# Performance work log

Measured on AMD Instinct MI355X. Metric: run time of the kernel, lower is better.

Reference implementation:

```python
import jax, jax.numpy as jnp
import numpy as np

B, C, H, W = 16, 256, 96, 96


def setup_inputs() -> dict:
    key = jax.random.key(0)
    ks = jax.random.split(key, 10)
    s = 1.0 / np.sqrt(C)
    return {
        "x": jax.random.normal(ks[0], (B, C, H, W), dtype=jnp.float32) * 0.1,
        "w_theta": jax.random.normal(ks[1], (C, C), dtype=jnp.float32) * s,
        "b_theta": jax.random.normal(ks[2], (C,), dtype=jnp.float32) * 0.01,
        "w_phi": jax.random.normal(ks[3], (C, C), dtype=jnp.float32) * s,
        "b_phi": jax.random.normal(ks[4], (C,), dtype=jnp.float32) * 0.01,
        "w_g": jax.random.normal(ks[5], (C, C), dtype=jnp.float32) * s,
        "b_g": jax.random.normal(ks[6], (C,), dtype=jnp.float32) * 0.01,
        "beta_w": jax.random.normal(ks[7], (), dtype=jnp.float32) * 0.1,
        "beta_h": jax.random.normal(ks[8], (), dtype=jnp.float32) * 0.1,
        "beta_c": jax.random.normal(ks[9], (), dtype=jnp.float32) * 0.1,
    }


def _conv1x1(x, w, b):
    # 1x1 conv == channel mixing: [B,C,H,W] x [O,C] -> [B,O,H,W]
    return jnp.einsum('bchw,oc->bohw', x, w) + b[None, :, None, None]


def _axis_att(q, k, v, perm):
    # perm maps [B,C,H,W] -> [B, axis, rest...]; attention over `axis`
    qp = jnp.transpose(q, perm)
    kp = jnp.transpose(k, perm)
    vp = jnp.transpose(v, perm)
    shp = vp.shape
    n = shp[1]
    qf = qp.reshape(shp[0], n, -1)
    kf = kp.reshape(shp[0], n, -1)
    vf = vp.reshape(shp[0], n, -1)
    att = jax.nn.softmax(jnp.einsum('bik,bjk->bij', qf, kf), axis=-1)  # [B,n,n]
    out = jnp.einsum('bij,bjk->bik', att, vf).reshape(shp)
    inv = np.argsort(perm)
    return jnp.transpose(out, inv)


def reference(x, w_theta, b_theta, w_phi, b_phi, w_g, b_g, beta_w, beta_h, beta_c):
    # width: perm (0,3,2,1); height: (0,2,1,3); channel: (0,1,2,3)
    perms = [(0, 3, 2, 1), (0, 2, 1, 3), (0, 1, 2, 3)]
    betas = [beta_w, beta_h, beta_c]
    for perm, beta in zip(perms, betas):
        theta_x = _conv1x1(x, w_theta, b_theta)
        phi_x = _conv1x1(x, w_phi, b_phi)
        g_x = _conv1x1(x, w_g, b_g)
        x_t = _axis_att(theta_x, phi_x, g_x, perm)
        x = x + x_t * beta
    return x
```

## Files before the change

### kernel.cpp

```cpp
#include <hip/hip_runtime.h>
#include <hip/hip_bf16.h>

using bf16 = __hip_bfloat16;
using short8 = __attribute__((ext_vector_type(8))) short;
using float4v = __attribute__((ext_vector_type(4))) float;

#define BM 64
#define BN 64
#define BK 32
#define LDSP 40

__device__ inline short f2b(float x) {
  bf16 h = __float2bfloat16(x);
  return __builtin_bit_cast(short, h);
}

__device__ inline int swz(int row, int g) { return (g ^ ((row >> 3) & 3)) * 8; }

template<int F32>
__device__ inline short8 ld8e(const void* base, long eoff) {
  short8 r;
  if constexpr (F32) {
    const float* f = (const float*)base + eoff;
    #pragma unroll
    for (int i = 0; i < 8; ++i) r[i] = f2b(f[i]);
  } else {
    r = *(const short8*)((const short*)base + eoff);
  }
  return r;
}

template<int AF, int BF, int EPI, int AF32, int BF32>
__global__ __launch_bounds__(256) void gemm_k(
    const void* __restrict__ Ag, const void* __restrict__ Bg,
    void* __restrict__ Cv, void* __restrict__ Cv2, const float* __restrict__ bias,
    const float* __restrict__ betaP, const float* __restrict__ resid,
    short* __restrict__ xbout,
    int M, int N, int K, int lda, int ldb, int ldc,
    long sA, long sB, long sC, int ksplit, int abdiv, int msplit, int swapxy)
{
  constexpr int SMEM_SHORTS = (EPI >= 4) ? (64 * 68 * 2) : ((BM + BN) * LDSP);
  __shared__ __align__(16) short smem[SMEM_SHORTS];
  short (*As)[LDSP] = (short (*)[LDSP])smem;
  short (*Bs)[LDSP] = (short (*)[LDSP])(smem + BM * LDSP);
  const int t = threadIdx.x;
  const int lane = t & 63;
  const int wave = t >> 6;
  const int wm = (wave >> 1) * 32;
  const int wn = (wave & 1) * 32;
  const int fr = lane & 15;
  const int fq = lane >> 4;
  const int bz = blockIdx.z;
  const int batch = bz / ksplit;
  const int kc = bz - batch * ksplit;
  const int Kc = K / ksplit;
  const int k0 = kc * Kc;
  int bxi = blockIdx.x, byi = blockIdx.y;
  if (swapxy) { int tmp = bxi; bxi = byi; byi = tmp; }
  const int tm0 = byi * BM;
  const int tn0 = bxi * BN;
  const long abase = (long)(batch / abdiv) * sA;
  const long bbase = (long)batch * sB;

  float4v acc[2][2] = {};

  for (int kk = 0; kk < Kc; kk += BK) {
    const int kbase = k0 + kk;
    if constexpr (AF == 0 || AF == 2) {
      int m = t >> 2;
      int kloc = (t & 3) * 8;
      int gk = kbase + kloc;
      short8 v = {};
      if (tm0 + m < M) {
        long off;
        if constexpr (AF == 0) off = abase + (long)(tm0 + m) * lda + gk;
        else                   off = abase + (long)(gk / 96) * 9216 + (long)(tm0 + m) * 96 + (gk % 96);
        v = ld8e<AF32>(Ag, off);
      }
      *(short8*)&As[m][swz(m, t & 3)] = v;
    } else {
      int m = t & 63;
      int kg = t >> 6;
      short8 v = {};
      if (tm0 + m < M) {
        #pragma unroll
        for (int j = 0; j < 8; ++j) {
          long off = abase + (long)(kbase + kg * 8 + j) * lda + tm0 + m;
          v[j] = AF32 ? f2b(((const float*)Ag)[off]) : ((const short*)Ag)[off];
        }
      }
      *(short8*)&As[m][swz(m, kg)] = v;
    }
    if constexpr (BF == 0 || BF == 2) {
      int n = t >> 2;
      int kloc = (t & 3) * 8;
      int gk = kbase + kloc;
      short8 v = {};
      if (tn0 + n < N) {
        long off;
        if constexpr (BF == 0) off = bbase + (long)(tn0 + n) * ldb + gk;
        else                   off = bbase + (long)(gk / 96) * 9216 + (long)(tn0 + n) * 96 + (gk % 96);
        v = ld8e<BF32>(Bg, off);
      }
      *(short8*)&Bs[n][swz(n, t & 3)] = v;
    } else {
      int n = t & 63;
      int kg = t >> 6;
      short8 v = {};
      if (tn0 + n < N) {
        #pragma unroll
        for (int j = 0; j < 8; ++j) {
          long off = bbase + (long)(kbase + kg * 8 + j) * ldb + tn0 + n;
          v[j] = BF32 ? f2b(((const float*)Bg)[off]) : ((const short*)Bg)[off];
        }
      }
      *(short8*)&Bs[n][swz(n, kg)] = v;
    }
    __syncthreads();
    short8 af[2], bfv[2];
    #pragma unroll
    for (int i = 0; i < 2; ++i) { int r = wm + i * 16 + fr; af[i] = *(const short8*)&As[r][swz(r, fq)]; }
    #pragma unroll
    for (int j = 0; j < 2; ++j) { int r = wn + j * 16 + fr; bfv[j] = *(const short8*)&Bs[r][swz(r, fq)]; }
    #pragma unroll
    for (int i = 0; i < 2; ++i)
      #pragma unroll
      for (int j = 0; j < 2; ++j)
        acc[i][j] = __builtin_amdgcn_mfma_f32_16x16x32_bf16(af[i], bfv[j], acc[i][j], 0, 0, 0);
    __syncthreads();
  }

  float beta = 0.0f;
  if constexpr (EPI >= 2) beta = *betaP;
  const long cb = (long)batch * sC;

  if constexpr (EPI == 1) {
    short* Cb = (short*)Cv;
    int rbase = tm0;
    if (Cv2 != nullptr && tm0 >= msplit) { Cb = (short*)Cv2; rbase = tm0 - msplit; }
    short (*Ct)[72] = (short (*)[72])smem;
    #pragma unroll
    for (int i = 0; i < 2; ++i)
      #pragma unroll
      for (int j = 0; j < 2; ++j)
        #pragma unroll
        for (int r = 0; r < 4; ++r) {
          int row = wm + i * 16 + fq * 4 + r;
          int col = wn + j * 16 + fr;
          float v = acc[i][j][r];
          if (bias) v += bias[tm0 + row];
          Ct[row][col] = f2b(v);
        }
    __syncthreads();
    const bool full = (tm0 + BM <= M) && (tn0 + BN <= N);
    #pragma unroll
    for (int rr = 0; rr < 2; ++rr) {
      int row = rr * 32 + (t >> 3);
      int c8 = (t & 7) * 8;
      if (full) {
        *(short8*)(Cb + cb + (long)(rbase + row) * ldc + tn0 + c8) = *(const short8*)&Ct[row][c8];
      } else if (tm0 + row < M) {
        #pragma unroll
        for (int e = 0; e < 8; ++e)
          if (tn0 + c8 + e < N)
            Cb[cb + (long)(rbase + row) * ldc + tn0 + c8 + e] = Ct[row][c8 + e];
      }
    }
  } else if constexpr (EPI >= 4) {
    float (*Cf)[68] = (float (*)[68])smem;
    #pragma unroll
    for (int i = 0; i < 2; ++i)
      #pragma unroll
      for (int j = 0; j < 2; ++j)
        #pragma unroll
        for (int r = 0; r < 4; ++r)
          Cf[wm + i * 16 + fq * 4 + r][wn + j * 16 + fr] = acc[i][j][r];
    __syncthreads();
    int row = t >> 2;
    int seg = (t & 3) * 16;
    int grow = tm0 + row;
    if (grow < M && seg < N - tn0) {
      float* xp = (float*)Cv;
      long base = cb + (long)grow * ldc + tn0 + seg;
      float4v nv[4];
      #pragma unroll
      for (int q = 0; q < 4; ++q) {
        float4v xv;
        if constexpr (EPI == 4) xv = *(const float4v*)(xp + base + q * 4);
        else                    xv = *(const float4v*)(resid + base + q * 4);
        #pragma unroll
        for (int e = 0; e < 4; ++e) nv[q][e] = xv[e] + beta * Cf[row][seg + q * 4 + e];
        *(float4v*)(xp + base + q * 4) = nv[q];
      }
      if (xbout) {
        short8 s0, s1;
        #pragma unroll
        for (int e = 0; e < 4; ++e) { s0[e] = f2b(nv[0][e]); s0[e + 4] = f2b(nv[1][e]); }
        #pragma unroll
        for (int e = 0; e < 4; ++e) { s1[e] = f2b(nv[2][e]); s1[e + 4] = f2b(nv[3][e]); }
        *(short8*)(xbout + base) = s0;
        *(short8*)(xbout + base + 8) = s1;
      }
    }
  } else {
    #pragma unroll
    for (int i = 0; i < 2; ++i) {
      #pragma unroll
      for (int j = 0; j < 2; ++j) {
        #pragma unroll
        for (int r = 0; r < 4; ++r) {
          int row = tm0 + wm + i * 16 + fq * 4 + r;
          int col = tn0 + wn + j * 16 + fr;
          if (row < M && col < N)
            atomicAdd((float*)Cv + cb + (long)row * ldc + col, acc[i][j][r]);
        }
      }
    }
  }
}

__global__ __launch_bounds__(256) void cvt_k(
    const float* __restrict__ in, short* __restrict__ out, long n)
{
  long i = ((long)blockIdx.x * 256 + threadIdx.x) * 8;
  if (i >= n) return;
  const float4v* p = (const float4v*)(in + i);
  float4v a = p[0], b = p[1];
  short8 v;
  v[0] = f2b(a[0]); v[1] = f2b(a[1]); v[2] = f2b(a[2]); v[3] = f2b(a[3]);
  v[4] = f2b(b[0]); v[5] = f2b(b[1]); v[6] = f2b(b[2]); v[7] = f2b(b[3]);
  *(short8*)(out + i) = v;
}

__global__ __launch_bounds__(256) void softmax_k(
    const float* __restrict__ in, short* __restrict__ out, int n, int rows,
    const float* __restrict__ addj, const float* __restrict__ rowv,
    const float* __restrict__ colv)
{
  int wave = threadIdx.x >> 6;
  int lane = threadIdx.x & 63;
  int row = blockIdx.x * 4 + wave;
  if (row >= rows) return;
  int b = row / n;
  const float* r = in + (long)row * n;
  float rv = rowv ? rowv[row] : 0.0f;
  float vals[4];
  float m = -1e30f;
  #pragma unroll
  for (int i = 0; i < 4; ++i) {
    int c = lane + i * 64;
    float v = -1e30f;
    if (c < n) {
      v = r[c];
      if (addj) v += addj[(long)b * n + c];
      if (colv) v += rv * colv[c];
    }
    vals[i] = v;
    m = fmaxf(m, v);
  }
  #pragma unroll
  for (int off = 32; off > 0; off >>= 1) m = fmaxf(m, __shfl_xor(m, off));
  float s = 0.0f;
  #pragma unroll
  for (int i = 0; i < 4; ++i) {
    int c = lane + i * 64;
    float e = (c < n) ? __expf(vals[i] - m) : 0.0f;
    vals[i] = e;
    s += e;
  }
  #pragma unroll
  for (int off = 32; off > 0; off >>= 1) s += __shfl_xor(s, off);
  float inv = 1.0f / s;
  #pragma unroll
  for (int i = 0; i < 4; ++i) {
    int c = lane + i * 64;
    if (c < n) out[(long)row * n + c] = f2b(vals[i] * inv);
  }
}

__global__ __launch_bounds__(256) void sum_rows_k(
    const short* __restrict__ src, float* __restrict__ dst, int rowlen, int nrows)
{
  int wave = threadIdx.x >> 6;
  int lane = threadIdx.x & 63;
  int row = blockIdx.x * 4 + wave;
  if (row >= nrows) return;
  const short* p = src + (long)row * rowlen;
  float s = 0.0f;
  for (int k = lane; k < rowlen; k += 64)
    s += __bfloat162float(__builtin_bit_cast(bf16, p[k]));
  #pragma unroll
  for (int off = 32; off > 0; off >>= 1) s += __shfl_xor(s, off);
  if (lane == 0) dst[row] = s;
}

__global__ __launch_bounds__(256) void wv_k(
    const float* __restrict__ wphi, const float* __restrict__ btheta, float* __restrict__ wv)
{
  int c = threadIdx.x;
  float s = 0.0f;
  for (int o = 0; o < 256; ++o) s += btheta[o] * wphi[o * 256 + c];
  wv[c] = s;
}

__global__ __launch_bounds__(256) void vfull_k(
    const float* __restrict__ x, const float* __restrict__ wv, float* __restrict__ vf)
{
  long idx = (long)blockIdx.x * 256 + threadIdx.x;
  int b = (int)(idx / 9216);
  int hw = (int)(idx % 9216);
  const float* p = x + (long)b * 2359296 + hw;
  float s = 0.0f;
  for (int c = 0; c < 256; ++c) s += wv[c] * p[(long)c * 9216];
  vf[idx] = s;
}

__global__ __launch_bounds__(256) void rsum_k(
    const float* __restrict__ vf, float* __restrict__ r, int axis)
{
  int idx = blockIdx.x * 256 + threadIdx.x;
  int b = idx / 96;
  int j = idx % 96;
  const float* p = vf + (long)b * 9216;
  float s = 0.0f;
  if (axis == 0) { for (int h = 0; h < 96; ++h) s += p[h * 96 + j]; }
  else           { for (int w = 0; w < 96; ++w) s += p[j * 96 + w]; }
  r[idx] = s;
}

__global__ __launch_bounds__(256) void fill_k(
    const float* __restrict__ wth, const float* __restrict__ wg,
    const float* __restrict__ bth, const float* __restrict__ bg,
    short* __restrict__ st1, short* __restrict__ st2,
    float* __restrict__ b1, float* __restrict__ b2)
{
  int r = blockIdx.x, c = threadIdx.x;
  if (r < 256) {
    st2[r * 256 + c] = f2b(wth[r * 256 + c]);
  } else {
    short v = f2b(wg[(r - 256) * 256 + c]);
    st1[r * 256 + c] = v;
    st2[r * 256 + c] = v;
  }
  if (r == 0) { b1[c] = 0.0f; b2[c] = bth[c]; }
  if (r == 1) { b1[256 + c] = bg[c]; b2[256 + c] = bg[c]; }
}

extern "C" void kernel_launch(void* const* d_in, const int* in_sizes, int n_in,
                              void* d_out, int out_size, void* d_ws, size_t ws_size,
                              hipStream_t stream)
{
  const long TS = 37748736L;
  const long BS = 2359296L;
  const size_t POOL = 12u * 1024 * 1024;

  float* x = (float*)d_out;
  const float* xin = (const float*)d_in[0];
  const float* wth = (const float*)d_in[1];
  const float* bth = (const float*)d_in[2];
  const float* wph = (const float*)d_in[3];
  const float* bph = (const float*)d_in[4];
  const float* wg  = (const float*)d_in[5];
  const float* bg  = (const float*)d_in[6];
  const float* beta_w = (const float*)d_in[7];
  const float* beta_h = (const float*)d_in[8];
  const float* beta_c = (const float*)d_in[9];

  const size_t need_full = (size_t)6 * TS + POOL;
  const bool full = ws_size >= need_full;

  short* xb   = (short*)d_ws;
  short* bigY = xb + TS;
  char*  pool = (char*)(bigY + TS);
  short* bigG = full ? (short*)(pool + POOL) : bigY;
  float* attf  = (float*)pool;
  short* attb  = (short*)(attf + 1048576);
  float* Zf    = (float*)(attb + 1048576);
  short* st1   = (short*)(Zf + 1048576);
  short* st2   = st1 + 131072;
  float* bias1 = (float*)(st2 + 131072);
  float* bias2 = bias1 + 512;
  float* vfull = bias2 + 512;
  float* rbuf  = vfull + 147456;
  float* wv    = rbuf + 1536;
  float* tbar  = wv + 256;

  dim3 blk(256);

  gemm_k<1,1,1,1,1><<<dim3(4,4,1), blk, 0, stream>>>(wth, wph, st1, nullptr, nullptr, nullptr, nullptr,
      nullptr, 256, 256, 256, 256, 256, 256, 0, 0, 0, 1, 1, 0, 0);
  fill_k<<<512, blk, 0, stream>>>(wth, wg, bth, bg, st1, st2, bias1, bias2);
  wv_k<<<1, blk, 0, stream>>>(wph, bth, wv);
  cvt_k<<<18432, blk, 0, stream>>>(xin, xb, TS);

  for (int pass = 0; pass < 2; ++pass) {
    const float* xs = (pass == 0) ? xin : (const float*)x;
    if (full) {
      gemm_k<0,1,1,0,0><<<dim3(144,8,16), blk, 0, stream>>>(st1, xb, bigY, bigG, bias1, nullptr, nullptr,
          nullptr, 512, 9216, 256, 256, 9216, 9216, 0, BS, BS, 1, 1, 256, 0);
    } else {
      gemm_k<0,1,1,0,0><<<dim3(144,4,16), blk, 0, stream>>>(st1, xb, bigY, nullptr, nullptr, nullptr, nullptr,
          nullptr, 256, 9216, 256, 256, 9216, 9216, 0, BS, BS, 1, 1, 0, 0);
    }
    vfull_k<<<576, blk, 0, stream>>>(xs, wv, vfull);
    rsum_k<<<6, blk, 0, stream>>>(vfull, rbuf, pass);
    hipMemsetAsync(attf, 0, (size_t)16 * 9216 * sizeof(float), stream);
    if (pass == 0)
      gemm_k<1,1,0,0,0><<<dim3(2,2,256), blk, 0, stream>>>(xb, bigY, attf, nullptr, nullptr, nullptr, nullptr,
          nullptr, 96, 96, 24576, 96, 96, 96, BS, BS, 9216, 16, 1, 0, 0);
    else
      gemm_k<2,2,0,0,0><<<dim3(2,2,256), blk, 0, stream>>>(xb, bigY, attf, nullptr, nullptr, nullptr, nullptr,
          nullptr, 96, 96, 24576, 0, 0, 96, BS, BS, 9216, 16, 1, 0, 0);
    softmax_k<<<384, blk, 0, stream>>>(attf, attb, 96, 1536, rbuf, nullptr, nullptr);
    if (!full) {
      gemm_k<0,1,1,0,0><<<dim3(144,4,16), blk, 0, stream>>>(st1 + 65536, xb, bigG, nullptr, bias1 + 256,
          nullptr, nullptr, nullptr, 256, 9216, 256, 256, 9216, 9216, 0, BS, BS, 1, 1, 0, 0);
    }
    if (pass == 0)
      gemm_k<0,0,5,0,0><<<dim3(2,384,16), blk, 0, stream>>>(bigG, attb, x, nullptr, nullptr, beta_w, xin,
          xb, 24576, 96, 96, 96, 96, 96, BS, 9216, BS, 1, 1, 0, 0);
    else
      gemm_k<0,1,4,0,0><<<dim3(2,2,4096), blk, 0, stream>>>(attb, bigG, x, nullptr, nullptr, beta_h, nullptr,
          xb, 96, 96, 96, 96, 96, 96, 9216, 9216, 9216, 1, 256, 0, 0);
  }

  if (full) {
    gemm_k<0,1,1,0,0><<<dim3(144,8,16), blk, 0, stream>>>(st2, xb, bigY, bigG, bias2, nullptr, nullptr,
        nullptr, 512, 9216, 256, 256, 9216, 9216, 0, BS, BS, 1, 1, 256, 0);
  } else {
    gemm_k<0,1,1,0,0><<<dim3(144,4,16), blk, 0, stream>>>(st2, xb, bigY, nullptr, bias2, nullptr, nullptr,
        nullptr, 256, 9216, 256, 256, 9216, 9216, 0, BS, BS, 1, 1, 0, 0);
  }
  hipMemsetAsync(Zf, 0, (size_t)16 * 256 * 256 * sizeof(float), stream);
  gemm_k<0,0,0,0,0><<<dim3(4,4,64), blk, 0, stream>>>(bigY, xb, Zf, nullptr, nullptr, nullptr, nullptr,
      nullptr, 256, 256, 9216, 9216, 9216, 256, BS, BS, 65536, 4, 1, 0, 0);
  sum_rows_k<<<1024, blk, 0, stream>>>(bigY, tbar, 9216, 4096);
  hipMemsetAsync(attf, 0, (size_t)16 * 256 * 256 * sizeof(float), stream);
  gemm_k<0,0,0,1,1><<<dim3(4,4,16), blk, 0, stream>>>(Zf, wph, attf, nullptr, nullptr, nullptr, nullptr,
      nullptr, 256, 256, 256, 256, 256, 256, 65536, 0, 65536, 1, 1, 0, 0);
  softmax_k<<<1024, blk, 0, stream>>>(attf, attb, 256, 4096, nullptr, tbar, bph);
  if (!full) {
    gemm_k<0,1,1,0,0><<<dim3(144,4,16), blk, 0, stream>>>(st1 + 65536, xb, bigG, nullptr, bias1 + 256,
        nullptr, nullptr, nullptr, 256, 9216, 256, 256, 9216, 9216, 0, BS, BS, 1, 1, 0, 0);
  }
  gemm_k<0,1,4,0,0><<<dim3(144,4,16), blk, 0, stream>>>(attb, bigG, x, nullptr, nullptr, beta_c, nullptr,
      nullptr, 256, 9216, 256, 256, 9216, 9216, 65536, BS, BS, 1, 1, 0, 0);
}
```

Before: 1.445 ms.

## Compute channel attention via Gram matrix of x instead of theta projection

The channel-attention logits theta·phiᵀ are re-associated as Wθ·(X Xᵀ)·Wφᵀ plus bias terms built from per-channel sums of x. The large theta projection GEMM over all pixels is replaced by a 256x256 Gram GEMM per batch followed by small weight GEMMs. The per-channel sums are accumulated with atomics inside the preceding height-pass epilogue, and rank-one bias corrections are folded into the initial logits. This drops the K=9216 projection and the row-sum kernel, at the cost of extra small kernels and a different rounding path through bf16 Gram storage.

Result: no change. 1.441 ms (-0.3%).

```diff
diff --git a/kernel.cpp b/kernel.cpp
--- a/kernel.cpp
+++ b/kernel.cpp
@@ -35,7 +35,7 @@
     const void* __restrict__ Ag, const void* __restrict__ Bg,
     void* __restrict__ Cv, void* __restrict__ Cv2, const float* __restrict__ bias,
     const float* __restrict__ betaP, const float* __restrict__ resid,
-    short* __restrict__ xbout,
+    short* __restrict__ xbout, float* __restrict__ xbarP,
     int M, int N, int K, int lda, int ldb, int ldc,
     long sA, long sB, long sC, int ksplit, int abdiv, int msplit, int swapxy)
 {
@@ -179,6 +179,7 @@
     int row = t >> 2;
     int seg = (t & 3) * 16;
     int grow = tm0 + row;
+    float part = 0.0f;
     if (grow < M && seg < N - tn0) {
       float* xp = (float*)Cv;
       long base = cb + (long)grow * ldc + tn0 + seg;
@@ -189,7 +190,7 @@
         if constexpr (EPI == 4) xv = *(const float4v*)(xp + base + q * 4);
         else                    xv = *(const float4v*)(resid + base + q * 4);
         #pragma unroll
-        for (int e = 0; e < 4; ++e) nv[q][e] = xv[e] + beta * Cf[row][seg + q * 4 + e];
+        for (int e = 0; e < 4; ++e) { nv[q][e] = xv[e] + beta * Cf[row][seg + q * 4 + e]; part += nv[q][e]; }
         *(float4v*)(xp + base + q * 4) = nv[q];
       }
       if (xbout) {
@@ -201,6 +202,11 @@
         *(short8*)(xbout + base) = s0;
         *(short8*)(xbout + base + 8) = s1;
       }
+    }
+    if (xbarP) {
+      #pragma unroll
+      for (int off = 32; off > 0; off >>= 1) part += __shfl_xor(part, off);
+      if (lane == 0) atomicAdd(&xbarP[batch], part);
     }
   } else {
     #pragma unroll
@@ -278,22 +284,6 @@
   }
 }
 
-__global__ __launch_bounds__(256) void sum_rows_k(
-    const short* __restrict__ src, float* __restrict__ dst, int rowlen, int nrows)
-{
-  int wave = threadIdx.x >> 6;
-  int lane = threadIdx.x & 63;
-  int row = blockIdx.x * 4 + wave;
-  if (row >= nrows) return;
-  const short* p = src + (long)row * rowlen;
-  float s = 0.0f;
-  for (int k = lane; k < rowlen; k += 64)
-    s += __bfloat162float(__builtin_bit_cast(bf16, p[k]));
-  #pragma unroll
-  for (int off = 32; off > 0; off >>= 1) s += __shfl_xor(s, off);
-  if (lane == 0) dst[row] = s;
-}
-
 __global__ __launch_bounds__(256) void wv_k(
     const float* __restrict__ wphi, const float* __restrict__ btheta, float* __restrict__ wv)
 {
@@ -326,6 +316,32 @@
   if (axis == 0) { for (int h = 0; h < 96; ++h) s += p[h * 96 + j]; }
   else           { for (int w = 0; w < 96; ++w) s += p[j * 96 + w]; }
   r[idx] = s;
+}
+
+__global__ __launch_bounds__(256) void tq_k(
+    const float* __restrict__ wth, const float* __restrict__ bth,
+    const float* __restrict__ wph, const float* __restrict__ xbar,
+    float* __restrict__ tbar, float* __restrict__ q)
+{
+  int b = blockIdx.x, i = threadIdx.x;
+  const float* xb_ = xbar + b * 256;
+  float s1 = 0.0f, s2 = 0.0f;
+  for (int k = 0; k < 256; ++k) {
+    s1 += wth[i * 256 + k] * xb_[k];
+    s2 += wph[i * 256 + k] * xb_[k];
+  }
+  tbar[b * 256 + i] = s1 + 9216.0f * bth[i];
+  q[b * 256 + i] = s2;
+}
+
+__global__ __launch_bounds__(256) void initL_k(
+    const float* __restrict__ tbar, const float* __restrict__ q,
+    const float* __restrict__ bth, const float* __restrict__ bph,
+    float* __restrict__ attf)
+{
+  int bi = blockIdx.x;
+  int b = bi >> 8, i = bi & 255, j = threadIdx.x;
+  attf[(long)bi * 256 + j] = tbar[bi] * bph[j] + bth[i] * q[b * 256 + j];
 }
 
 __global__ __launch_bounds__(256) void fill_k(
@@ -384,65 +400,62 @@
   float* rbuf  = vfull + 147456;
   float* wv    = rbuf + 1536;
   float* tbar  = wv + 256;
+  float* xbar  = tbar + 4096;
+  float* qv    = xbar + 4096;
+  short* Sb    = attb;
+  short* Ztb   = (short*)Zf;
 
   dim3 blk(256);
 
   gemm_k<1,1,1,1,1><<<dim3(4,4,1), blk, 0, stream>>>(wth, wph, st1, nullptr, nullptr, nullptr, nullptr,
-      nullptr, 256, 256, 256, 256, 256, 256, 0, 0, 0, 1, 1, 0, 0);
+      nullptr, nullptr, 256, 256, 256, 256, 256, 256, 0, 0, 0, 1, 1, 0, 0);
   fill_k<<<512, blk, 0, stream>>>(wth, wg, bth, bg, st1, st2, bias1, bias2);
   wv_k<<<1, blk, 0, stream>>>(wph, bth, wv);
   cvt_k<<<18432, blk, 0, stream>>>(xin, xb, TS);
+  hipMemsetAsync(xbar, 0, 4096 * sizeof(float), stream);
 
   for (int pass = 0; pass < 2; ++pass) {
     const float* xs = (pass == 0) ? xin : (const float*)x;
     if (full) {
       gemm_k<0,1,1,0,0><<<dim3(144,8,16), blk, 0, stream>>>(st1, xb, bigY, bigG, bias1, nullptr, nullptr,
-          nullptr, 512, 9216, 256, 256, 9216, 9216, 0, BS, BS, 1, 1, 256, 0);
+          nullptr, nullptr, 512, 9216, 256, 256, 9216, 9216, 0, BS, BS, 1, 1, 256, 0);
     } else {
       gemm_k<0,1,1,0,0><<<dim3(144,4,16), blk, 0, stream>>>(st1, xb, bigY, nullptr, nullptr, nullptr, nullptr,
-          nullptr, 256, 9216, 256, 256, 9216, 9216, 0, BS, BS, 1, 1, 0, 0);
+          nullptr, nullptr, 256, 9216, 256, 256, 9216, 9216, 0, BS, BS, 1, 1, 0, 0);
     }
     vfull_k<<<576, blk, 0, stream>>>(xs, wv, vfull);
     rsum_k<<<6, blk, 0, stream>>>(vfull, rbuf, pass);
     hipMemsetAsync(attf, 0, (size_t)16 * 9216 * sizeof(float), stream);
     if (pass == 0)
       gemm_k<1,1,0,0,0><<<dim3(2,2,256), blk, 0, stream>>>(xb, bigY, attf, nullptr, nullptr, nullptr, nullptr,
-          nullptr, 96, 96, 24576, 96, 96, 96, BS, BS, 9216, 16, 1, 0, 0);
+          nullptr, nullptr, 96, 96, 24576, 96, 96, 96, BS, BS, 9216, 16, 1, 0, 0);
     else
       gemm_k<2,2,0,0,0><<<dim3(2,2,256), blk, 0, stream>>>(xb, bigY, attf, nullptr, nullptr, nullptr, nullptr,
-          nullptr, 96, 96, 24576, 0, 0, 96, BS, BS, 9216, 16, 1, 0, 0);
+          nullptr, nullptr, 96, 96, 24576, 0, 0, 96, BS, BS, 9216, 16, 1, 0, 0);
     softmax_k<<<384, blk, 0, stream>>>(attf, attb, 96, 1536, rbuf, nullptr, nullptr);
     if (!full) {
       gemm_k<0,1,1,0,0><<<dim3(144,4,16), blk, 0, stream>>>(st1 + 65536, xb, bigG, nullptr, bias1 + 256,
-          nullptr, nullptr, nullptr, 256, 9216, 256, 256, 9216, 9216, 0, BS, BS, 1, 1, 0, 0);
+          nullptr, nullptr, nullptr, nullptr, 256, 9216, 256, 256, 9216, 9216, 0, BS, BS, 1, 1, 0, 0);
     }
     if (pass == 0)
       gemm_k<0,0,5,0,0><<<dim3(2,384,16), blk, 0, stream>>>(bigG, attb, x, nullptr, nullptr, beta_w, xin,
-          xb, 24576, 96, 96, 96, 96, 96, BS, 9216, BS, 1, 1, 0, 0);
+          xb, nullptr, 24576, 96, 96, 96, 96, 96, BS, 9216, BS, 1, 1, 0, 0);
     else
       gemm_k<0,1,4,0,0><<<dim3(2,2,4096), blk, 0, stream>>>(attb, bigG, x, nullptr, nullptr, beta_h, nullptr,
-          xb, 96, 96, 96, 96, 96, 96, 9216, 9216, 9216, 1, 256, 0, 0);
-  }
-
-  if (full) {
-    gemm_k<0,1,1,0,0><<<dim3(144,8,16), blk, 0, stream>>>(st2, xb, bigY, bigG, bias2, nullptr, nullptr,
-        nullptr, 512, 9216, 256, 256, 9216, 9216, 0, BS, BS, 1, 1, 256, 0);
-  } else {
-    gemm_k<0,1,1,0,0><<<dim3(144,4,16), blk, 0, stream>>>(st2, xb, bigY, nullptr, bias2, nullptr, nullptr,
-        nullptr, 256, 9216, 256, 256, 9216, 9216, 0, BS, BS, 1, 1, 0, 0);
-  }
-  hipMemsetAsync(Zf, 0, (size_t)16 * 256 * 256 * sizeof(float), stream);
-  gemm_k<0,0,0,0,0><<<dim3(4,4,64), blk, 0, stream>>>(bigY, xb, Zf, nullptr, nullptr, nullptr, nullptr,
-      nullptr, 256, 256, 9216, 9216, 9216, 256, BS, BS, 65536, 4, 1, 0, 0);
-  sum_rows_k<<<1024, blk, 0, stream>>>(bigY, tbar, 9216, 4096);
-  hipMemsetAsync(attf, 0, (size_t)16 * 256 * 256 * sizeof(float), stream);
-  gemm_k<0,0,0,1,1><<<dim3(4,4,16), blk, 0, stream>>>(Zf, wph, attf, nullptr, nullptr, nullptr, nullptr,
-      nullptr, 256, 256, 256, 256, 256, 256, 65536, 0, 65536, 1, 1, 0, 0);
-  softmax_k<<<1024, blk, 0, stream>>>(attf, attb, 256, 4096, nullptr, tbar, bph);
-  if (!full) {
-    gemm_k<0,1,1,0,0><<<dim3(144,4,16), blk, 0, stream>>>(st1 + 65536, xb, bigG, nullptr, bias1 + 256,
-        nullptr, nullptr, nullptr, 256, 9216, 256, 256, 9216, 9216, 0, BS, BS, 1, 1, 0, 0);
-  }
+          xb, xbar, 96, 96, 96, 96, 96, 96, 9216, 9216, 9216, 1, 256, 0, 0);
+  }
+
+  gemm_k<0,1,1,0,0><<<dim3(144,4,16), blk, 0, stream>>>(st1 + 65536, xb, bigG, nullptr, bias1 + 256,
+      nullptr, nullptr, nullptr, nullptr, 256, 9216, 256, 256, 9216, 9216, 0, BS, BS, 1, 1, 0, 0);
+  gemm_k<0,0,1,0,0><<<dim3(4,4,16), blk, 0, stream>>>(xb, xb, Sb, nullptr, nullptr, nullptr, nullptr,
+      nullptr, nullptr, 256, 256, 9216, 9216, 9216, 256, BS, BS, 65536, 1, 1, 0, 0);
+  gemm_k<0,0,1,1,0><<<dim3(4,4,16), blk, 0, stream>>>(wth, Sb, Ztb, nullptr, nullptr, nullptr, nullptr,
+      nullptr, nullptr, 256, 256, 256, 256, 256, 256, 0, 65536, 65536, 1, 1, 0, 0);
+  tq_k<<<16, blk, 0, stream>>>(wth, bth, wph, xbar, tbar, qv);
+  initL_k<<<4096, blk, 0, stream>>>(tbar, qv, bth, bph, attf);
+  gemm_k<0,0,0,0,1><<<dim3(4,4,16), blk, 0, stream>>>(Ztb, wph, attf, nullptr, nullptr, nullptr, nullptr,
+      nullptr, nullptr, 256, 256, 256, 256, 256, 256, 65536, 0, 65536, 1, 1, 0, 0);
+  softmax_k<<<1024, blk, 0, stream>>>(attf, attb, 256, 4096, nullptr, nullptr, nullptr);
   gemm_k<0,1,4,0,0><<<dim3(144,4,16), blk, 0, stream>>>(attb, bigG, x, nullptr, nullptr, beta_c, nullptr,
-      nullptr, 256, 9216, 256, 256, 9216, 9216, 65536, BS, BS, 1, 1, 0, 0);
-}
+      nullptr, nullptr, 256, 9216, 256, 256, 9216, 9216, 65536, BS, BS, 1, 1, 0, 0);
+}
```
